# Kernel optimization log

Measured on AMD Instinct MI355X. Metric: run time of the kernel, lower is better.

Reference implementation:

```python
import jax, jax.numpy as jnp
import numpy as np

DIM = 1024
HEADS = 16
DIM_HEAD = 64
INNER = HEADS * DIM_HEAD
LN_EPS = 1e-5


def setup_inputs() -> dict:
    key = jax.random.key(0)
    ks = jax.random.split(key, 6)
    b, n = 2, 2048
    x = jax.random.normal(ks[0], (b, n, DIM), dtype=jnp.float32)
    attn_bias = jax.random.normal(ks[1], (HEADS, n, n), dtype=jnp.float32)
    # learned params
    ln_gamma = jnp.ones((DIM,), dtype=jnp.float32)
    ln_beta = jnp.zeros((DIM,), dtype=jnp.float32)
    w_qkv = jax.random.normal(ks[2], (DIM, 3 * INNER), dtype=jnp.float32) / np.sqrt(DIM)
    w_out = jax.random.normal(ks[3], (INNER, DIM), dtype=jnp.float32) / np.sqrt(INNER)
    return {"x": x, "attn_bias": attn_bias, "ln_gamma": ln_gamma,
            "ln_beta": ln_beta, "w_qkv": w_qkv, "w_out": w_out}


def reference(x, attn_bias, ln_gamma, ln_beta, w_qkv, w_out):
    b, n, _ = x.shape
    scale = DIM_HEAD ** -0.5
    # LayerNorm
    mu = jnp.mean(x, axis=-1, keepdims=True)
    var = jnp.mean(jnp.square(x - mu), axis=-1, keepdims=True)
    xn = (x - mu) * jax.lax.rsqrt(var + LN_EPS) * ln_gamma + ln_beta
    # QKV projection: [b, n, 3*inner]
    qkv = xn @ w_qkv
    q, k, v = jnp.split(qkv, 3, axis=-1)
    # [b, n, inner] -> [b, h, n, d]
    split_heads = lambda t: t.reshape(b, n, HEADS, DIM_HEAD).transpose(0, 2, 1, 3)
    q, k, v = split_heads(q) * scale, split_heads(k), split_heads(v)
    sim = jnp.einsum('bhid,bhjd->bhij', q, k)
    sim = sim + attn_bias[None]  # broadcast over batch
    mask_value = -jnp.finfo(sim.dtype).max
    causal = jnp.triu(jnp.ones((n, n), dtype=bool), k=1)
    sim = jnp.where(causal, mask_value, sim)
    attn = jax.nn.softmax(sim, axis=-1)
    out = jnp.einsum('bhij,bhjd->bhid', attn, v)
    out = out.transpose(0, 2, 1, 3).reshape(b, n, INNER)
    return out @ w_out
```

## Files before the change

kernel.cpp:

```cpp
#include <hip/hip_runtime.h>
#include <hip/hip_bf16.h>
#include <math.h>

typedef unsigned short u16;
typedef __attribute__((ext_vector_type(8))) __bf16 bf16x8;
typedef __attribute__((ext_vector_type(4))) float f32x4;

static __device__ __forceinline__ u16 f2bf(float f) {
    unsigned int u = __builtin_bit_cast(unsigned int, f);
    u += 0x7fffu + ((u >> 16) & 1u);
    return (u16)(u >> 16);
}

__global__ __launch_bounds__(256) void ln_kernel(
    const float* __restrict__ x, const float* __restrict__ g,
    const float* __restrict__ bta, u16* __restrict__ xn)
{
    const int row = blockIdx.x;
    const int tid = threadIdx.x;
    const float4 v = *(const float4*)&x[(size_t)row * 1024 + tid * 4];
    float s  = v.x + v.y + v.z + v.w;
    float s2 = v.x * v.x + v.y * v.y + v.z * v.z + v.w * v.w;
    #pragma unroll
    for (int off = 32; off; off >>= 1) {
        s  += __shfl_xor(s,  off);
        s2 += __shfl_xor(s2, off);
    }
    __shared__ float red[8];
    if ((tid & 63) == 0) { red[tid >> 6] = s; red[4 + (tid >> 6)] = s2; }
    __syncthreads();
    s  = red[0] + red[1] + red[2] + red[3];
    s2 = red[4] + red[5] + red[6] + red[7];
    const float mean = s * (1.0f / 1024.0f);
    const float var  = s2 * (1.0f / 1024.0f) - mean * mean;
    const float rstd = rsqrtf(var + 1e-5f);
    const float4 gg = *(const float4*)&g[tid * 4];
    const float4 bb = *(const float4*)&bta[tid * 4];
    ushort4 o;
    o.x = f2bf((v.x - mean) * rstd * gg.x + bb.x);
    o.y = f2bf((v.y - mean) * rstd * gg.y + bb.y);
    o.z = f2bf((v.z - mean) * rstd * gg.z + bb.z);
    o.w = f2bf((v.w - mean) * rstd * gg.w + bb.w);
    *(ushort4*)&xn[(size_t)row * 1024 + tid * 4] = o;
}

__global__ __launch_bounds__(256) void transpose_w(
    const float* __restrict__ in, u16* __restrict__ outT, int K, int N)
{
    const int k0 = blockIdx.x * 64, n0 = blockIdx.y * 64;
    const int tid = threadIdx.x;
    __shared__ u16 tile[64][72];
    #pragma unroll
    for (int i = 0; i < 4; ++i) {
        int c = tid + i * 256;
        int kr = c >> 4, nc = (c & 15) * 4;
        float4 v = *(const float4*)&in[(size_t)(k0 + kr) * N + n0 + nc];
        tile[nc + 0][kr] = f2bf(v.x);
        tile[nc + 1][kr] = f2bf(v.y);
        tile[nc + 2][kr] = f2bf(v.z);
        tile[nc + 3][kr] = f2bf(v.w);
    }
    __syncthreads();
    #pragma unroll
    for (int i = 0; i < 4; ++i) {
        int c = tid + i * 256;
        int nr = c >> 4, kc = (c & 15) * 4;
        ushort4 w = *(const ushort4*)&tile[nr][kc];
        *(ushort4*)&outT[(size_t)(n0 + nr) * K + k0 + kc] = w;
    }
}

__global__ __launch_bounds__(256) void transpose_v_kernel(
    const u16* __restrict__ V, u16* __restrict__ Vt)
{
    const int bh = blockIdx.y;
    const int n0 = blockIdx.x * 64;
    const int tid = threadIdx.x;
    __shared__ u16 t[64][72];
    #pragma unroll
    for (int i = 0; i < 2; ++i) {
        int c = tid + (i << 8);
        int nr = c >> 3, dc = (c & 7) * 8;
        int4 v4 = *(const int4*)&V[((size_t)bh * 2048 + n0 + nr) * 64 + dc];
        union { int4 v; u16 u[8]; } uu; uu.v = v4;
        #pragma unroll
        for (int j = 0; j < 8; ++j) t[dc + j][nr] = uu.u[j];
    }
    __syncthreads();
    #pragma unroll
    for (int i = 0; i < 2; ++i) {
        int c = tid + (i << 8);
        int d = c >> 3, nn = (c & 7) * 8;
        int4 v4 = *(const int4*)&t[d][nn];
        *(int4*)&Vt[((size_t)bh * 64 + d) * 2048 + n0 + nn] = v4;
    }
}

template <int EPI>
__global__ __launch_bounds__(256) void gemm_bf16_k(
    const u16* __restrict__ A, const u16* __restrict__ Bt,
    int M, int N, int K,
    float* __restrict__ Cf,
    u16* __restrict__ Qo, u16* __restrict__ Ko, u16* __restrict__ Vo)
{
    __shared__ u16 lds[2][8192];
    const int tid = threadIdx.x;
    const int lane = tid & 63, w = tid >> 6;
    const int l15 = lane & 15, l4 = lane >> 4;
    const int wm = w & 1, wn = w >> 1;
    const int n0 = blockIdx.x * 128, m0 = blockIdx.y * 128;

    auto stage = [&](int buf, int kt) {
        const u16* Ab = A + (size_t)m0 * K + kt * 32;
        const u16* Bb = Bt + (size_t)n0 * K + kt * 32;
        #pragma unroll
        for (int i = 0; i < 2; ++i) {
            int c = tid + (i << 8);
            int r = c >> 2, ke = (c & 3) * 8;
            __builtin_amdgcn_global_load_lds(
                (const __attribute__((address_space(1))) void*)(Ab + (size_t)r * K + ke),
                (__attribute__((address_space(3))) void*)(&lds[buf][0] + c * 8), 16, 0, 0);
            __builtin_amdgcn_global_load_lds(
                (const __attribute__((address_space(1))) void*)(Bb + (size_t)r * K + ke),
                (__attribute__((address_space(3))) void*)(&lds[buf][4096] + c * 8), 16, 0, 0);
        }
    };

    f32x4 acc[4][4];
    #pragma unroll
    for (int mf = 0; mf < 4; ++mf)
        #pragma unroll
        for (int nf = 0; nf < 4; ++nf)
            acc[mf][nf] = f32x4{0.f, 0.f, 0.f, 0.f};

    const int NT = K >> 5;
    stage(0, 0);
    __syncthreads();
    for (int kt = 0; kt < NT; ++kt) {
        const int buf = kt & 1;
        if (kt + 1 < NT) stage(buf ^ 1, kt + 1);
        const u16* Ab = &lds[buf][0];
        const u16* Bb = &lds[buf][4096];
        bf16x8 af[4], bfv[4];
        #pragma unroll
        for (int mf = 0; mf < 4; ++mf)
            af[mf] = *(const bf16x8*)(Ab + (wm * 64 + mf * 16 + l15) * 32 + l4 * 8);
        #pragma unroll
        for (int nf = 0; nf < 4; ++nf)
            bfv[nf] = *(const bf16x8*)(Bb + (wn * 64 + nf * 16 + l15) * 32 + l4 * 8);
        #pragma unroll
        for (int mf = 0; mf < 4; ++mf)
            #pragma unroll
            for (int nf = 0; nf < 4; ++nf)
                acc[mf][nf] = __builtin_amdgcn_mfma_f32_16x16x32_bf16(
                    af[mf], bfv[nf], acc[mf][nf], 0, 0, 0);
        __syncthreads();
    }

    #pragma unroll
    for (int mf = 0; mf < 4; ++mf) {
        #pragma unroll
        for (int nf = 0; nf < 4; ++nf) {
            #pragma unroll
            for (int r = 0; r < 4; ++r) {
                const int row = m0 + wm * 64 + mf * 16 + l4 * 4 + r;
                const int col = n0 + wn * 64 + nf * 16 + l15;
                const float v = acc[mf][nf][r];
                if (EPI == 1) {
                    Cf[(size_t)row * N + col] = v;
                } else {
                    const int t = col >> 10, rem = col & 1023;
                    const int h = rem >> 6, d = rem & 63;
                    const int b = row >> 11, nn = row & 2047;
                    const size_t idx = ((size_t)((b * 16 + h) * 2048 + nn)) * 64 + d;
                    if (t == 0)      Qo[idx] = f2bf(v * 0.125f);
                    else if (t == 1) Ko[idx] = f2bf(v);
                    else             Vo[idx] = f2bf(v);
                }
            }
        }
    }
}

__global__ __launch_bounds__(512, 4) void attn_kernel(
    const u16* __restrict__ Q, const u16* __restrict__ Kmat,
    const u16* __restrict__ Vt, const float* __restrict__ bias,
    u16* __restrict__ att)
{
    const int hb = blockIdx.x;
    const int h = hb >> 1, b = hb & 1;
    const int bh = b * 16 + h;
    const int y = blockIdx.y;
    const int qb = (y < 8) ? y : 23 - y;
    const int q0 = qb << 7;
    const int tid = threadIdx.x;
    const int w = tid >> 6, lane = tid & 63;
    const int l15 = lane & 15, l4 = lane >> 4;

    __shared__ u16 K_lds[2][64][72];
    __shared__ u16 V_lds[2][64][72];
    __shared__ u16 P_lds[8][16][72];

    const int qrow_a = q0 + w * 16 + l15;
    bf16x8 qa[2];
    #pragma unroll
    for (int ks = 0; ks < 2; ++ks)
        qa[ks] = *(const bf16x8*)(Q + ((size_t)bh * 2048 + qrow_a) * 64 + ks * 32 + l4 * 8);

    f32x4 acc_o[4];
    #pragma unroll
    for (int nf = 0; nf < 4; ++nf) acc_o[nf] = f32x4{0.f, 0.f, 0.f, 0.f};
    float m_r[4], l_r[4];
    #pragma unroll
    for (int r = 0; r < 4; ++r) { m_r[r] = -INFINITY; l_r[r] = 0.f; }

    const int qrow_c = q0 + w * 16 + l4 * 4;
    const float* biasrow = bias + (size_t)h * 2048 * 2048;

    const int rr_s = tid >> 3, pp_s = (tid & 7) * 8;
    int4 kreg, vreg;
    auto issue_loads = [&](int j0n) {
        kreg = *(const int4*)&Kmat[((size_t)bh * 2048 + j0n + rr_s) * 64 + pp_s];
        vreg = *(const int4*)&Vt[((size_t)bh * 64 + rr_s) * 2048 + j0n + pp_s];
    };
    issue_loads(0);

    const int NT = 2 * qb + 2;
    for (int jt = 0; jt < NT; ++jt) {
        const int j0 = jt << 6;
        const int buf = jt & 1;
        *(int4*)&K_lds[buf][rr_s][pp_s] = kreg;
        *(int4*)&V_lds[buf][rr_s][pp_s] = vreg;
        if (jt + 1 < NT) issue_loads(j0 + 64);
        float breg[4][4];
        #pragma unroll
        for (int nf = 0; nf < 4; ++nf)
            #pragma unroll
            for (int r = 0; r < 4; ++r)
                breg[nf][r] = biasrow[(size_t)(qrow_c + r) * 2048 + j0 + nf * 16 + l15];
        __syncthreads();

        if (j0 > q0 + w * 16 + 15) continue;

        f32x4 s[4];
        #pragma unroll
        for (int nf = 0; nf < 4; ++nf) s[nf] = f32x4{0.f, 0.f, 0.f, 0.f};
        __builtin_amdgcn_s_setprio(1);
        #pragma unroll
        for (int ks = 0; ks < 2; ++ks)
            #pragma unroll
            for (int nf = 0; nf < 4; ++nf) {
                bf16x8 kb = *(const bf16x8*)&K_lds[buf][nf * 16 + l15][ks * 32 + l4 * 8];
                s[nf] = __builtin_amdgcn_mfma_f32_16x16x32_bf16(qa[ks], kb, s[nf], 0, 0, 0);
            }
        __builtin_amdgcn_s_setprio(0);

        float sv[4][4];
        if (j0 + 63 > q0 + w * 16) {
            #pragma unroll
            for (int nf = 0; nf < 4; ++nf) {
                const int col = j0 + nf * 16 + l15;
                #pragma unroll
                for (int r = 0; r < 4; ++r) {
                    const int qr = qrow_c + r;
                    float v = s[nf][r] + breg[nf][r];
                    sv[nf][r] = (col > qr) ? -1e30f : v;
                }
            }
        } else {
            #pragma unroll
            for (int nf = 0; nf < 4; ++nf)
                #pragma unroll
                for (int r = 0; r < 4; ++r)
                    sv[nf][r] = s[nf][r] + breg[nf][r];
        }

        float mt[4];
        #pragma unroll
        for (int r = 0; r < 4; ++r)
            mt[r] = fmaxf(fmaxf(sv[0][r], sv[1][r]), fmaxf(sv[2][r], sv[3][r]));
        int need = 0;
        #pragma unroll
        for (int r = 0; r < 4; ++r) need |= (mt[r] > m_r[r] + 8.0f);
        if (__any(need)) {
            #pragma unroll
            for (int off = 1; off < 16; off <<= 1)
                #pragma unroll
                for (int r = 0; r < 4; ++r) mt[r] = fmaxf(mt[r], __shfl_xor(mt[r], off));
            #pragma unroll
            for (int r = 0; r < 4; ++r) {
                const float mn = fmaxf(m_r[r], mt[r]);
                const float alpha = __expf(m_r[r] - mn);
                m_r[r] = mn;
                l_r[r] *= alpha;
                #pragma unroll
                for (int nf = 0; nf < 4; ++nf) acc_o[nf][r] *= alpha;
            }
        }

        float pv_[4][4], ps[4] = {0.f, 0.f, 0.f, 0.f};
        #pragma unroll
        for (int nf = 0; nf < 4; ++nf)
            #pragma unroll
            for (int r = 0; r < 4; ++r) {
                const float pp = __expf(sv[nf][r] - m_r[r]);
                pv_[nf][r] = pp;
                ps[r] += pp;
            }
        #pragma unroll
        for (int off = 1; off < 16; off <<= 1)
            #pragma unroll
            for (int r = 0; r < 4; ++r) ps[r] += __shfl_xor(ps[r], off);
        #pragma unroll
        for (int r = 0; r < 4; ++r) l_r[r] += ps[r];

        #pragma unroll
        for (int nf = 0; nf < 4; ++nf)
            #pragma unroll
            for (int r = 0; r < 4; ++r)
                P_lds[w][l4 * 4 + r][nf * 16 + l15] = f2bf(pv_[nf][r]);

        __builtin_amdgcn_s_setprio(1);
        #pragma unroll
        for (int ks = 0; ks < 2; ++ks) {
            bf16x8 pa = *(const bf16x8*)&P_lds[w][l15][ks * 32 + l4 * 8];
            #pragma unroll
            for (int nf = 0; nf < 4; ++nf) {
                bf16x8 vb = *(const bf16x8*)&V_lds[buf][nf * 16 + l15][ks * 32 + l4 * 8];
                acc_o[nf] = __builtin_amdgcn_mfma_f32_16x16x32_bf16(pa, vb, acc_o[nf], 0, 0, 0);
            }
        }
        __builtin_amdgcn_s_setprio(0);
    }

    #pragma unroll
    for (int nf = 0; nf < 4; ++nf)
        #pragma unroll
        for (int r = 0; r < 4; ++r) {
            const int qr = qrow_c + r;
            const float o = acc_o[nf][r] / l_r[r];
            att[((size_t)b * 2048 + qr) * 1024 + h * 64 + nf * 16 + l15] = f2bf(o);
        }
}

extern "C" void kernel_launch(void* const* d_in, const int* in_sizes, int n_in,
                              void* d_out, int out_size, void* d_ws, size_t ws_size,
                              hipStream_t stream) {
    const float* x     = (const float*)d_in[0];
    const float* bias  = (const float*)d_in[1];
    const float* gamma = (const float*)d_in[2];
    const float* beta_ = (const float*)d_in[3];
    const float* wqkv  = (const float*)d_in[4];
    const float* wout  = (const float*)d_in[5];
    float* out = (float*)d_out;

    char* ws = (char*)d_ws;
    u16* xn     = (u16*)(ws + 0);
    u16* wqkvT  = (u16*)(ws + 8388608);
    u16* woutT  = (u16*)(ws + 14680064);
    u16* Qb     = (u16*)(ws + 16777216);
    u16* Kb     = (u16*)(ws + 25165824);
    u16* Vb     = (u16*)(ws + 33554432);
    u16* Vtb    = (u16*)(ws + 41943040);
    u16* attb   = xn;

    ln_kernel<<<4096, 256, 0, stream>>>(x, gamma, beta_, xn);
    transpose_w<<<dim3(16, 48), 256, 0, stream>>>(wqkv, wqkvT, 1024, 3072);
    transpose_w<<<dim3(16, 16), 256, 0, stream>>>(wout, woutT, 1024, 1024);
    gemm_bf16_k<0><<<dim3(24, 32), 256, 0, stream>>>(xn, wqkvT, 4096, 3072, 1024,
                                                     nullptr, Qb, Kb, Vb);
    transpose_v_kernel<<<dim3(32, 32), 256, 0, stream>>>(Vb, Vtb);
    attn_kernel<<<dim3(32, 16), 512, 0, stream>>>(Qb, Kb, Vtb, bias, attb);
    gemm_bf16_k<1><<<dim3(8, 32), 256, 0, stream>>>(attb, woutT, 4096, 1024, 1024,
                                                    out, nullptr, nullptr, nullptr);
}
```

Before: 152.1 us.

## Prefetch next tile's bias and K/V during compute in attention loop

Restructures the attention key loop so that the next tile's K/V global loads and the bias loads are issued right after the barrier and overlap with the current tile's MFMA and softmax work. The LDS store for the next buffer moves to the end of the step, and the bias uses ping-pong register arrays via a manually 2x-unrolled loop. It also skips bias loads for tiles fully masked for the wave. Trade-off: more live registers (two bias arrays plus prefetch regs), which may lower occupancy.

```diff
diff --git a/kernel.cpp b/kernel.cpp
--- a/kernel.cpp
+++ b/kernel.cpp
@@ -215,6 +215,7 @@
     for (int r = 0; r < 4; ++r) { m_r[r] = -INFINITY; l_r[r] = 0.f; }
 
     const int qrow_c = q0 + w * 16 + l4 * 4;
+    const int qlim = q0 + w * 16 + 15;
     const float* biasrow = bias + (size_t)h * 2048 * 2048;
 
     const int rr_s = tid >> 3, pp_s = (tid & 7) * 8;
@@ -223,114 +224,132 @@
         kreg = *(const int4*)&Kmat[((size_t)bh * 2048 + j0n + rr_s) * 64 + pp_s];
         vreg = *(const int4*)&Vt[((size_t)bh * 64 + rr_s) * 2048 + j0n + pp_s];
     };
+    auto load_bias = [&](int j0n, float (&dst)[4][4]) {
+        #pragma unroll
+        for (int nf = 0; nf < 4; ++nf)
+            #pragma unroll
+            for (int r = 0; r < 4; ++r)
+                dst[nf][r] = biasrow[(size_t)(qrow_c + r) * 2048 + j0n + nf * 16 + l15];
+    };
+
+    const int NT = 2 * qb + 2;
+    float bregA[4][4], bregB[4][4];
+
     issue_loads(0);
-
-    const int NT = 2 * qb + 2;
-    for (int jt = 0; jt < NT; ++jt) {
+    load_bias(0, bregA);
+    *(int4*)&K_lds[0][rr_s][pp_s] = kreg;
+    *(int4*)&V_lds[0][rr_s][pp_s] = vreg;
+
+    auto tile_step = [&](int jt, float (&bcur)[4][4], float (&bnext)[4][4]) {
         const int j0 = jt << 6;
         const int buf = jt & 1;
-        *(int4*)&K_lds[buf][rr_s][pp_s] = kreg;
-        *(int4*)&V_lds[buf][rr_s][pp_s] = vreg;
-        if (jt + 1 < NT) issue_loads(j0 + 64);
-        float breg[4][4];
-        #pragma unroll
-        for (int nf = 0; nf < 4; ++nf)
+        __syncthreads();
+        if (jt + 1 < NT) {
+            issue_loads((jt + 1) << 6);
+            if (((jt + 1) << 6) <= qlim) load_bias((jt + 1) << 6, bnext);
+        }
+
+        if (j0 <= qlim) {
+            f32x4 s[4];
+            #pragma unroll
+            for (int nf = 0; nf < 4; ++nf) s[nf] = f32x4{0.f, 0.f, 0.f, 0.f};
+            __builtin_amdgcn_s_setprio(1);
+            #pragma unroll
+            for (int ks = 0; ks < 2; ++ks)
+                #pragma unroll
+                for (int nf = 0; nf < 4; ++nf) {
+                    bf16x8 kb = *(const bf16x8*)&K_lds[buf][nf * 16 + l15][ks * 32 + l4 * 8];
+                    s[nf] = __builtin_amdgcn_mfma_f32_16x16x32_bf16(qa[ks], kb, s[nf], 0, 0, 0);
+                }
+            __builtin_amdgcn_s_setprio(0);
+
+            float sv[4][4];
+            if (j0 + 63 > q0 + w * 16) {
+                #pragma unroll
+                for (int nf = 0; nf < 4; ++nf) {
+                    const int col = j0 + nf * 16 + l15;
+                    #pragma unroll
+                    for (int r = 0; r < 4; ++r) {
+                        const int qr = qrow_c + r;
+                        float v = s[nf][r] + bcur[nf][r];
+                        sv[nf][r] = (col > qr) ? -1e30f : v;
+                    }
+                }
+            } else {
+                #pragma unroll
+                for (int nf = 0; nf < 4; ++nf)
+                    #pragma unroll
+                    for (int r = 0; r < 4; ++r)
+                        sv[nf][r] = s[nf][r] + bcur[nf][r];
+            }
+
+            float mt[4];
             #pragma unroll
             for (int r = 0; r < 4; ++r)
-                breg[nf][r] = biasrow[(size_t)(qrow_c + r) * 2048 + j0 + nf * 16 + l15];
-        __syncthreads();
-
-        if (j0 > q0 + w * 16 + 15) continue;
-
-        f32x4 s[4];
-        #pragma unroll
-        for (int nf = 0; nf < 4; ++nf) s[nf] = f32x4{0.f, 0.f, 0.f, 0.f};
-        __builtin_amdgcn_s_setprio(1);
-        #pragma unroll
-        for (int ks = 0; ks < 2; ++ks)
-            #pragma unroll
-            for (int nf = 0; nf < 4; ++nf) {
-                bf16x8 kb = *(const bf16x8*)&K_lds[buf][nf * 16 + l15][ks * 32 + l4 * 8];
-                s[nf] = __builtin_amdgcn_mfma_f32_16x16x32_bf16(qa[ks], kb, s[nf], 0, 0, 0);
+                mt[r] = fmaxf(fmaxf(sv[0][r], sv[1][r]), fmaxf(sv[2][r], sv[3][r]));
+            int need = 0;
+            #pragma unroll
+            for (int r = 0; r < 4; ++r) need |= (mt[r] > m_r[r] + 8.0f);
+            if (__any(need)) {
+                #pragma unroll
+                for (int off = 1; off < 16; off <<= 1)
+                    #pragma unroll
+                    for (int r = 0; r < 4; ++r) mt[r] = fmaxf(mt[r], __shfl_xor(mt[r], off));
+                #pragma unroll
+                for (int r = 0; r < 4; ++r) {
+                    const float mn = fmaxf(m_r[r], mt[r]);
+                    const float alpha = __expf(m_r[r] - mn);
+                    m_r[r] = mn;
+                    l_r[r] *= alpha;
+                    #pragma unroll
+                    for (int nf = 0; nf < 4; ++nf) acc_o[nf][r] *= alpha;
+                }
             }
-        __builtin_amdgcn_s_setprio(0);
-
-        float sv[4][4];
-        if (j0 + 63 > q0 + w * 16) {
-            #pragma unroll
-            for (int nf = 0; nf < 4; ++nf) {
-                const int col = j0 + nf * 16 + l15;
+
+            float pv_[4][4], ps[4] = {0.f, 0.f, 0.f, 0.f};
+            #pragma unroll
+            for (int nf = 0; nf < 4; ++nf)
                 #pragma unroll
                 for (int r = 0; r < 4; ++r) {
-                    const int qr = qrow_c + r;
-                    float v = s[nf][r] + breg[nf][r];
-                    sv[nf][r] = (col > qr) ? -1e30f : v;
+                    const float pp = __expf(sv[nf][r] - m_r[r]);
+                    pv_[nf][r] = pp;
+                    ps[r] += pp;
+                }
+            #pragma unroll
+            for (int off = 1; off < 16; off <<= 1)
+                #pragma unroll
+                for (int r = 0; r < 4; ++r) ps[r] += __shfl_xor(ps[r], off);
+            #pragma unroll
+            for (int r = 0; r < 4; ++r) l_r[r] += ps[r];
+
+            #pragma unroll
+            for (int nf = 0; nf < 4; ++nf)
+                #pragma unroll
+                for (int r = 0; r < 4; ++r)
+                    P_lds[w][l4 * 4 + r][nf * 16 + l15] = f2bf(pv_[nf][r]);
+
+            __builtin_amdgcn_s_setprio(1);
+            #pragma unroll
+            for (int ks = 0; ks < 2; ++ks) {
+                bf16x8 pa = *(const bf16x8*)&P_lds[w][l15][ks * 32 + l4 * 8];
+                #pragma unroll
+                for (int nf = 0; nf < 4; ++nf) {
+                    bf16x8 vb = *(const bf16x8*)&V_lds[buf][nf * 16 + l15][ks * 32 + l4 * 8];
+                    acc_o[nf] = __builtin_amdgcn_mfma_f32_16x16x32_bf16(pa, vb, acc_o[nf], 0, 0, 0);
                 }
             }
-        } else {
-            #pragma unroll
-            for (int nf = 0; nf < 4; ++nf)
-                #pragma unroll
-                for (int r = 0; r < 4; ++r)
-                    sv[nf][r] = s[nf][r] + breg[nf][r];
-        }
-
-        float mt[4];
-        #pragma unroll
-        for (int r = 0; r < 4; ++r)
-            mt[r] = fmaxf(fmaxf(sv[0][r], sv[1][r]), fmaxf(sv[2][r], sv[3][r]));
-        int need = 0;
-        #pragma unroll
-        for (int r = 0; r < 4; ++r) need |= (mt[r] > m_r[r] + 8.0f);
-        if (__any(need)) {
-            #pragma unroll
-            for (int off = 1; off < 16; off <<= 1)
-                #pragma unroll
-                for (int r = 0; r < 4; ++r) mt[r] = fmaxf(mt[r], __shfl_xor(mt[r], off));
-            #pragma unroll
-            for (int r = 0; r < 4; ++r) {
-                const float mn = fmaxf(m_r[r], mt[r]);
-                const float alpha = __expf(m_r[r] - mn);
-                m_r[r] = mn;
-                l_r[r] *= alpha;
-                #pragma unroll
-                for (int nf = 0; nf < 4; ++nf) acc_o[nf][r] *= alpha;
-            }
-        }
-
-        float pv_[4][4], ps[4] = {0.f, 0.f, 0.f, 0.f};
-        #pragma unroll
-        for (int nf = 0; nf < 4; ++nf)
-            #pragma unroll
-            for (int r = 0; r < 4; ++r) {
-                const float pp = __expf(sv[nf][r] - m_r[r]);
-                pv_[nf][r] = pp;
-                ps[r] += pp;
-            }
-        #pragma unroll
-        for (int off = 1; off < 16; off <<= 1)
-            #pragma unroll
-            for (int r = 0; r < 4; ++r) ps[r] += __shfl_xor(ps[r], off);
-        #pragma unroll
-        for (int r = 0; r < 4; ++r) l_r[r] += ps[r];
-
-        #pragma unroll
-        for (int nf = 0; nf < 4; ++nf)
-            #pragma unroll
-            for (int r = 0; r < 4; ++r)
-                P_lds[w][l4 * 4 + r][nf * 16 + l15] = f2bf(pv_[nf][r]);
-
-        __builtin_amdgcn_s_setprio(1);
-        #pragma unroll
-        for (int ks = 0; ks < 2; ++ks) {
-            bf16x8 pa = *(const bf16x8*)&P_lds[w][l15][ks * 32 + l4 * 8];
-            #pragma unroll
-            for (int nf = 0; nf < 4; ++nf) {
-                bf16x8 vb = *(const bf16x8*)&V_lds[buf][nf * 16 + l15][ks * 32 + l4 * 8];
-                acc_o[nf] = __builtin_amdgcn_mfma_f32_16x16x32_bf16(pa, vb, acc_o[nf], 0, 0, 0);
-            }
-        }
-        __builtin_amdgcn_s_setprio(0);
+            __builtin_amdgcn_s_setprio(0);
+        }
+
+        if (jt + 1 < NT) {
+            *(int4*)&K_lds[buf ^ 1][rr_s][pp_s] = kreg;
+            *(int4*)&V_lds[buf ^ 1][rr_s][pp_s] = vreg;
+        }
+    };
+
+    for (int jt = 0; jt < NT; jt += 2) {
+        tile_step(jt,     bregA, bregB);
+        tile_step(jt + 1, bregB, bregA);
     }
 
     #pragma unroll
```

Result: slower. 226.3 us (+48.8%).
